# Performance work log

Measured on AMD Instinct MI355X. Metric: run time of the kernel, lower is better.

Reference implementation:

```python
import jax, jax.numpy as jnp
import numpy as np

B, T, D = 4, 1024, 1024
H, DK, DV = 4, 256, 512  # head_k_dim=256, head_v_dim=head_dim*expand_v=512
K_CONV = 4
EPS = 1e-5
L2_EPS = 1e-6


def silu(x):
    return x * jax.nn.sigmoid(x)


def causal_dw_conv(x, w):
    # x: [B,T,C], w: [C,K] depthwise causal conv (torch conv1d groups=C, left pad K-1)
    Kk = w.shape[1]
    xp = jnp.pad(x, ((0, 0), (Kk - 1, 0), (0, 0)))
    Tlen = x.shape[1]
    out = jnp.zeros_like(x)
    for i in range(Kk):
        out = out + xp[:, i:i + Tlen, :] * w[:, i]
    return out


def l2norm(x):
    return x * jax.lax.rsqrt(jnp.sum(x * x, axis=-1, keepdims=True) + L2_EPS)


def setup_inputs() -> dict:
    key = jax.random.key(0)
    ks = jax.random.split(key, 16)
    s = 0.02
    inp = {
        'x': jax.random.normal(ks[0], (B, T, D), jnp.float32),
        'Wq': jax.random.normal(ks[1], (D, H * DK), jnp.float32) * s,
        'Wk': jax.random.normal(ks[2], (D, H * DK), jnp.float32) * s,
        'Wv': jax.random.normal(ks[3], (D, H * DV), jnp.float32) * s,
        'conv_q_w': jax.random.normal(ks[4], (H * DK, K_CONV), jnp.float32) * 0.3,
        'conv_k_w': jax.random.normal(ks[5], (H * DK, K_CONV), jnp.float32) * 0.3,
        'conv_v_w': jax.random.normal(ks[6], (H * DV, K_CONV), jnp.float32) * 0.3,
        'Wb': jax.random.normal(ks[7], (D, H), jnp.float32) * s,
        'Wa': jax.random.normal(ks[8], (D, H), jnp.float32) * s,
        'A_log': jnp.log(jax.random.uniform(ks[9], (H,), jnp.float32, 1.0, 16.0)),
        'dt_bias': jax.random.normal(ks[10], (H,), jnp.float32) * 0.5,
        'Wg': jax.random.normal(ks[11], (D, H * DV), jnp.float32) * s,
        'norm_w': jnp.ones((DV,), jnp.float32),
        'Wo': jax.random.normal(ks[12], (H * DV, D), jnp.float32) * s,
    }
    return inp


def _forward(x, Wq, Wk, Wv, conv_q_w, conv_k_w, conv_v_w, Wb, Wa, A_log, dt_bias, Wg, norm_w, Wo):
    # projections + causal short conv + silu
    q = silu(causal_dw_conv(x @ Wq, conv_q_w)).reshape(B, T, H, DK)
    k = silu(causal_dw_conv(x @ Wk, conv_k_w)).reshape(B, T, H, DK)
    v = silu(causal_dw_conv(x @ Wv, conv_v_w)).reshape(B, T, H, DV)
    beta = jax.nn.sigmoid(x @ Wb)                                  # [B,T,H]
    g = -jnp.exp(A_log) * jax.nn.softplus(x @ Wa + dt_bias)        # [B,T,H]
    q = l2norm(q)
    k = l2norm(k)
    scale = DK ** -0.5

    # gated delta rule recurrence over time (state S: [B,H,DK,DV])
    qt = jnp.moveaxis(q, 1, 0)
    kt = jnp.moveaxis(k, 1, 0)
    vt = jnp.moveaxis(v, 1, 0)
    gt = jnp.moveaxis(g, 1, 0)
    bt = jnp.moveaxis(beta, 1, 0)

    S0 = jnp.zeros((B, H, DK, DV), x.dtype)

    def step(S, inps):
        q_t, k_t, v_t, g_t, b_t = inps
        S = S * jnp.exp(g_t)[..., None, None]
        kv = jnp.einsum('bhk,bhkv->bhv', k_t, S)
        delta = (v_t - kv) * b_t[..., None]
        S = S + jnp.einsum('bhk,bhv->bhkv', k_t, delta)
        o_t = jnp.einsum('bhk,bhkv->bhv', q_t * scale, S)
        return S, o_t

    _, o = jax.lax.scan(step, S0, (qt, kt, vt, gt, bt))
    o = jnp.moveaxis(o, 0, 1)                                      # [B,T,H,DV]

    # gated RMSNorm: rmsnorm(o) * weight * silu(gate)
    gate = (x @ Wg).reshape(B, T, H, DV)
    o = o * jax.lax.rsqrt(jnp.mean(o * o, axis=-1, keepdims=True) + EPS)
    o = o * norm_w * silu(gate)

    return o.reshape(B, T, H * DV) @ Wo


def reference(x, Wq, Wk, Wv, conv_q_w, conv_k_w, conv_v_w, Wb, Wa, A_log, dt_bias, Wg, norm_w, Wo):
    return _forward(x, Wq, Wk, Wv, conv_q_w, conv_k_w, conv_v_w, Wb, Wa, A_log, dt_bias, Wg, norm_w, Wo)
```

## Files before the change

kernel.cpp:

```cpp
#include <hip/hip_runtime.h>
#include <hip/hip_bf16.h>
#include <math.h>

#define B_ 4
#define T_ 1024
#define D_ 1024
#define H_ 4
#define DK_ 256
#define DV_ 512
#define KC_ 4

typedef __attribute__((ext_vector_type(4))) float floatx4;
typedef __attribute__((ext_vector_type(8))) short short8_t;

__device__ __forceinline__ unsigned short f2b(float f) {
    __hip_bfloat16 h = __float2bfloat16(f);
    return *(unsigned short*)&h;
}
__device__ __forceinline__ float b2f(unsigned short u) {
    unsigned int x = ((unsigned int)u) << 16;
    return *(float*)&x;
}

__global__ __launch_bounds__(256) void tob16_kernel(const float* __restrict__ in,
                                                    unsigned short* __restrict__ out) {
    int i = blockIdx.x * 256 + threadIdx.x;
    float4 f = ((const float4*)in)[i];
    ushort4 u;
    u.x = f2b(f.x); u.y = f2b(f.y); u.z = f2b(f.z); u.w = f2b(f.w);
    ((ushort4*)out)[i] = u;
}

__global__ __launch_bounds__(256) void transpose_bf16_kernel(const float* __restrict__ W,
                                                             unsigned short* __restrict__ Wt,
                                                             int K, int N) {
    __shared__ float Ls[32][33];
    int tx = threadIdx.x & 31, ty = threadIdx.x >> 5;
    int k0 = blockIdx.y * 32, n0 = blockIdx.x * 32;
#pragma unroll
    for (int i = 0; i < 4; ++i)
        Ls[ty * 4 + i][tx] = W[(size_t)(k0 + ty * 4 + i) * N + n0 + tx];
    __syncthreads();
#pragma unroll
    for (int i = 0; i < 4; ++i)
        Wt[(size_t)(n0 + ty * 4 + i) * K + k0 + tx] = f2b(Ls[tx][ty * 4 + i]);
}

__global__ __launch_bounds__(256) void gemm_bf16_kernel(const unsigned short* __restrict__ A,
                                                        const unsigned short* __restrict__ Bt,
                                                        float* __restrict__ C,
                                                        int M, int N, int K) {
    __shared__ unsigned short As[128 * 40];
    __shared__ unsigned short Bs[128 * 40];
    int tid = threadIdx.x;
    int m0 = blockIdx.y * 128, n0 = blockIdx.x * 128;
    int w = tid >> 6, lane = tid & 63;
    int wm = w >> 1, wn = w & 1;
    floatx4 acc[4][4] = {};

    int c0 = tid, c1 = 256 + tid;
    int r0 = c0 >> 2, col0 = (c0 & 3) * 8;
    int r1 = c1 >> 2, col1 = (c1 & 3) * 8;
    int koff = (lane >> 4) * 8;

    for (int k0 = 0; k0 < K; k0 += 32) {
        short8_t a0 = *(const short8_t*)&A[(size_t)(m0 + r0) * K + k0 + col0];
        short8_t a1 = *(const short8_t*)&A[(size_t)(m0 + r1) * K + k0 + col1];
        short8_t b0 = *(const short8_t*)&Bt[(size_t)(n0 + r0) * K + k0 + col0];
        short8_t b1 = *(const short8_t*)&Bt[(size_t)(n0 + r1) * K + k0 + col1];
        __syncthreads();
        *(short8_t*)&As[r0 * 40 + col0] = a0;
        *(short8_t*)&As[r1 * 40 + col1] = a1;
        *(short8_t*)&Bs[r0 * 40 + col0] = b0;
        *(short8_t*)&Bs[r1 * 40 + col1] = b1;
        __syncthreads();
        short8_t af[4], bf[4];
#pragma unroll
        for (int f = 0; f < 4; ++f) {
            af[f] = *(const short8_t*)&As[(wm * 64 + f * 16 + (lane & 15)) * 40 + koff];
            bf[f] = *(const short8_t*)&Bs[(wn * 64 + f * 16 + (lane & 15)) * 40 + koff];
        }
#pragma unroll
        for (int i = 0; i < 4; ++i)
#pragma unroll
            for (int j = 0; j < 4; ++j)
                acc[i][j] = __builtin_amdgcn_mfma_f32_16x16x32_bf16(af[i], bf[j], acc[i][j], 0, 0, 0);
    }
#pragma unroll
    for (int i = 0; i < 4; ++i) {
        int row = m0 + wm * 64 + i * 16 + (lane >> 4) * 4;
#pragma unroll
        for (int j = 0; j < 4; ++j) {
            int col = n0 + wn * 64 + j * 16 + (lane & 15);
#pragma unroll
            for (int r = 0; r < 4; ++r)
                C[(size_t)(row + r) * N + col] = acc[i][j][r];
        }
    }
}

__global__ __launch_bounds__(256) void betag_kernel(const float* __restrict__ x,
                                                    const float* __restrict__ Wb,
                                                    const float* __restrict__ Wa,
                                                    const float* __restrict__ A_log,
                                                    const float* __restrict__ dt_bias,
                                                    float* __restrict__ beta,
                                                    float* __restrict__ g) {
    int row = blockIdx.x;
    int tid = threadIdx.x;
    const float* xr = x + (size_t)row * D_;
    float pb[H_] = {}, pa[H_] = {};
    for (int j = 0; j < D_ / 256; ++j) {
        int d = j * 256 + tid;
        float xv = xr[d];
#pragma unroll
        for (int h = 0; h < H_; ++h) {
            pb[h] = fmaf(xv, Wb[d * H_ + h], pb[h]);
            pa[h] = fmaf(xv, Wa[d * H_ + h], pa[h]);
        }
    }
#pragma unroll
    for (int h = 0; h < H_; ++h) {
        for (int off = 32; off; off >>= 1) {
            pb[h] += __shfl_down(pb[h], off);
            pa[h] += __shfl_down(pa[h], off);
        }
    }
    __shared__ float ws[4][2][H_];
    int lane = tid & 63, w = tid >> 6;
    if (lane == 0) {
#pragma unroll
        for (int h = 0; h < H_; ++h) {
            ws[w][0][h] = pb[h];
            ws[w][1][h] = pa[h];
        }
    }
    __syncthreads();
    if (tid < H_) {
        float db = ws[0][0][tid] + ws[1][0][tid] + ws[2][0][tid] + ws[3][0][tid];
        float da = ws[0][1][tid] + ws[1][1][tid] + ws[2][1][tid] + ws[3][1][tid];
        beta[(size_t)row * H_ + tid] = 1.f / (1.f + expf(-db));
        float z = da + dt_bias[tid];
        float sp = (z > 20.f) ? z : log1pf(expf(z));
        g[(size_t)row * H_ + tid] = -expf(A_log[tid]) * sp;
    }
}

__global__ __launch_bounds__(256) void convqk_kernel(const float* __restrict__ raw,
                                                     const float* __restrict__ w,
                                                     __hip_bfloat16* __restrict__ out) {
    int bt_h = blockIdx.x;
    int h = bt_h & (H_ - 1);
    int row = bt_h >> 2;
    int t = row & (T_ - 1);
    int c = threadIdx.x;
    int C = h * DK_ + c;
    float acc = 0.f;
#pragma unroll
    for (int i = 0; i < KC_; ++i) {
        int tt = t - (KC_ - 1) + i;
        if (tt >= 0)
            acc = fmaf(raw[(size_t)(row - (KC_ - 1) + i) * (H_ * DK_) + C], w[C * KC_ + i], acc);
    }
    float s = acc / (1.f + expf(-acc));
    float ss = s * s;
    for (int off = 32; off; off >>= 1) ss += __shfl_down(ss, off);
    __shared__ float ws4[4];
    int lane = threadIdx.x & 63, wv = threadIdx.x >> 6;
    if (lane == 0) ws4[wv] = ss;
    __syncthreads();
    float tot = ws4[0] + ws4[1] + ws4[2] + ws4[3];
    float r = rsqrtf(tot + 1e-6f);
    out[(size_t)bt_h * DK_ + c] = __float2bfloat16(s * r);
}

__global__ __launch_bounds__(256) void convv_kernel(const float* __restrict__ raw,
                                                    const float* __restrict__ w,
                                                    __hip_bfloat16* __restrict__ out) {
    size_t idx = (size_t)blockIdx.x * 256 + threadIdx.x;
    int C = idx & (H_ * DV_ - 1);
    int row = (int)(idx >> 11);
    int t = row & (T_ - 1);
    float acc = 0.f;
#pragma unroll
    for (int i = 0; i < KC_; ++i) {
        int tt = t - (KC_ - 1) + i;
        if (tt >= 0)
            acc = fmaf(raw[(size_t)(row - (KC_ - 1) + i) * (H_ * DV_) + C], w[C * KC_ + i], acc);
    }
    out[idx] = __float2bfloat16(acc / (1.f + expf(-acc)));
}

__global__ __launch_bounds__(256) void prep_kernel(const unsigned short* __restrict__ qn,
                                                   const unsigned short* __restrict__ kn,
                                                   const float* __restrict__ gl,
                                                   const float* __restrict__ betal,
                                                   float* __restrict__ Afg,
                                                   unsigned short* __restrict__ KdTg,
                                                   unsigned short* __restrict__ Pg,
                                                   float* __restrict__ lambg,
                                                   float* __restrict__ scl0,
                                                   float* __restrict__ scl1) {
    int blk = blockIdx.x;
    int nc = blk & 31, bh = blk >> 5;
    int b = bh >> 2, h = bh & 3;
    int t0 = nc * 32;
    int tid = threadIdx.x, w = tid >> 6, l = tid & 63;
    int vl = l & 15, hq = l >> 4;
    size_t cb = (size_t)bh * 32 + nc;

    __shared__ __align__(16) unsigned short Kt[32][264];
    __shared__ float gcs[32], bets[32], kdec[32];

    if (tid < 32) {
        size_t base = ((size_t)(b * T_ + t0 + tid) * H_ + h);
        float gv = gl[base];
        float bv = betal[base];
        float x = gv;
#pragma unroll
        for (int off = 1; off < 32; off <<= 1) {
            float y = __shfl_up(x, off);
            if (tid >= off) x += y;
        }
        gcs[tid] = x;
        float lm = expf(x);
        bets[tid] = bv;
        float tot = __shfl(x, 31);
        kdec[tid] = expf(tot - x);
        lambg[cb * 32 + tid] = lm;
        scl0[cb * 32 + tid] = bv * lm;
        scl1[cb * 32 + tid] = bv;
    }
    __syncthreads();
    {
        int r = tid >> 3, c8 = (tid & 7) * 32;
        size_t gbase = ((size_t)(b * T_ + t0 + r) * H_ + h) * DK_;
#pragma unroll
        for (int ii = 0; ii < 4; ++ii)
            *(short8_t*)&Kt[r][c8 + ii * 8] = *(const short8_t*)&kn[gbase + c8 + ii * 8];
    }
    __syncthreads();
    if (w < 3) {
        int mt = (w == 0) ? 0 : 1;
        int nt = (w == 2) ? 1 : 0;
        floatx4 acc = {};
#pragma unroll
        for (int k0 = 0; k0 < 8; ++k0) {
            short8_t a = *(const short8_t*)&Kt[mt * 16 + vl][k0 * 32 + hq * 8];
            short8_t bb = *(const short8_t*)&Kt[nt * 16 + vl][k0 * 32 + hq * 8];
            acc = __builtin_amdgcn_mfma_f32_16x16x32_bf16(a, bb, acc, 0, 0, 0);
        }
#pragma unroll
        for (int r = 0; r < 4; ++r) {
            int i = mt * 16 + 4 * hq + r, j = nt * 16 + vl;
            Afg[cb * 1024 + i * 32 + j] = (j < i) ? bets[i] * expf(gcs[i] - gcs[j]) * acc[r] : 0.f;
        }
        floatx4 accp = {};
#pragma unroll
        for (int k0 = 0; k0 < 8; ++k0) {
            size_t qrow = ((size_t)(b * T_ + t0 + mt * 16 + vl) * H_ + h) * DK_ + k0 * 32 + hq * 8;
            short8_t a = *(const short8_t*)&qn[qrow];
            short8_t bb = *(const short8_t*)&Kt[nt * 16 + vl][k0 * 32 + hq * 8];
            accp = __builtin_amdgcn_mfma_f32_16x16x32_bf16(a, bb, accp, 0, 0, 0);
        }
#pragma unroll
        for (int r = 0; r < 4; ++r) {
            int i = mt * 16 + 4 * hq + r, j = nt * 16 + vl;
            Pg[cb * 1024 + i * 32 + j] = f2b((j <= i) ? expf(gcs[i] - gcs[j]) * accp[r] : 0.f);
        }
    } else {
#pragma unroll
        for (int ii = 0; ii < 4; ++ii)
            Pg[cb * 1024 + (l >> 2) * 32 + 16 + (l & 3) * 4 + ii] = 0;
    }
    {
#pragma unroll
        for (int it = 0; it < 16; ++it) {
            int uidx = it * 256 + tid;
            int k = uidx >> 4, cp = (uidx & 15) * 2;
            float kv0 = b2f(Kt[cp][k]) * kdec[cp];
            float kv1 = b2f(Kt[cp + 1][k]) * kdec[cp + 1];
            unsigned int pk = (unsigned int)f2b(kv0) | ((unsigned int)f2b(kv1) << 16);
            ((unsigned int*)KdTg)[cb * 4096 + uidx] = pk;
        }
    }
}

__global__ __launch_bounds__(256) void solve_kernel(const unsigned short* __restrict__ kn,
                                                    const unsigned short* __restrict__ vn,
                                                    const float* __restrict__ Afg,
                                                    const float* __restrict__ scl0,
                                                    const float* __restrict__ scl1,
                                                    unsigned short* __restrict__ Wpg,
                                                    unsigned short* __restrict__ Ug) {
    int part = blockIdx.x;
    int cbi = blockIdx.y;
    int bh = cbi >> 5, nc = cbi & 31;
    int b = bh >> 2, h = bh & 3;
    int t0 = nc * 32;
    int tid = threadIdx.x;

    __shared__ float Af[32][33];
    __shared__ float s0[32];
#pragma unroll
    for (int i = 0; i < 4; ++i) {
        int e = i * 256 + tid;
        Af[e >> 5][e & 31] = Afg[(size_t)cbi * 1024 + e];
    }
    if (tid < 32)
        s0[tid] = (part == 0) ? scl0[(size_t)cbi * 32 + tid] : scl1[(size_t)cbi * 32 + tid];
    __syncthreads();

    float u[32];
    if (part == 0) {
#pragma unroll
        for (int r = 0; r < 32; ++r)
            u[r] = s0[r] * b2f(kn[((size_t)(b * T_ + t0 + r) * H_ + h) * DK_ + tid]);
    } else {
        int col = (part - 1) * 256 + tid;
#pragma unroll
        for (int r = 0; r < 32; ++r)
            u[r] = s0[r] * b2f(vn[((size_t)(b * T_ + t0 + r) * H_ + h) * DV_ + col]);
    }
#pragma unroll
    for (int r = 1; r < 32; ++r) {
        float a = 0.f;
#pragma unroll
        for (int l2 = 0; l2 < r; ++l2)
            a = fmaf(Af[r][l2], u[l2], a);
        u[r] -= a;
    }
    if (part == 0) {
#pragma unroll
        for (int r = 0; r < 32; ++r)
            Wpg[(size_t)cbi * 8192 + r * 256 + tid] = f2b(u[r]);
    } else {
        int col = (part - 1) * 256 + tid;
#pragma unroll
        for (int r = 0; r < 32; ++r)
            Ug[((size_t)cbi * 32 + r) * 512 + col] = f2b(u[r]);
    }
}

__global__ __launch_bounds__(256) void seq_kernel(const unsigned short* __restrict__ qn,
                                                  const unsigned short* __restrict__ Wpg,
                                                  const unsigned short* __restrict__ KdTg,
                                                  const unsigned short* __restrict__ Pg,
                                                  const unsigned short* __restrict__ Ug,
                                                  const float* __restrict__ lambg,
                                                  float* __restrict__ o) {
    int blk = blockIdx.x;
    int vg = blk & 31, bh = blk >> 5;
    int b = bh >> 2, h = bh & 3;
    int tid = threadIdx.x;
    int w = tid >> 6, l = tid & 63;
    int vl = l & 15, hq = l >> 4;
    int v0 = vg * 16;

    __shared__ float Pu[4][32][17];
    __shared__ float Po[4][32][17];
    __shared__ __align__(16) unsigned short Ru[16][40];
    __shared__ float R2[4][64][17];

    float S[2][8] = {};

    for (int nc = 0; nc < 32; ++nc) {
        size_t cb = (size_t)bh * 32 + nc;
        int t0 = nc * 32;
        int ur_row = 8 * w + 2 * hq;
        float Ur0 = b2f(Ug[(cb * 32 + ur_row) * 512 + v0 + vl]);
        float Ur1 = b2f(Ug[(cb * 32 + ur_row + 1) * 512 + v0 + vl]);
        float lamC = lambg[cb * 32 + 31];
        float lmb[4];
        if (w < 2) {
#pragma unroll
            for (int r = 0; r < 4; ++r)
                lmb[r] = lambg[cb * 32 + 16 * w + 4 * hq + r];
        }
        short8_t bhi[2], blo[2];
#pragma unroll
        for (int kt = 0; kt < 2; ++kt)
#pragma unroll
            for (int j = 0; j < 8; ++j) {
                float sv = S[kt][j];
                unsigned short hh = f2b(sv);
                bhi[kt][j] = (short)hh;
                blo[kt][j] = (short)f2b(sv - b2f(hh));
            }
        floatx4 ua0 = {}, ua1 = {}, oa0 = {}, oa1 = {};
        const unsigned short* Wpc = Wpg + cb * 8192;
#pragma unroll
        for (int kt = 0; kt < 2; ++kt) {
            int kofs = w * 64 + kt * 32 + hq * 8;
            short8_t wa0 = *(const short8_t*)&Wpc[vl * 256 + kofs];
            short8_t wa1 = *(const short8_t*)&Wpc[(16 + vl) * 256 + kofs];
            short8_t qa0 = *(const short8_t*)&qn[((size_t)(b * T_ + t0 + vl) * H_ + h) * DK_ + kofs];
            short8_t qa1 = *(const short8_t*)&qn[((size_t)(b * T_ + t0 + 16 + vl) * H_ + h) * DK_ + kofs];
            ua0 = __builtin_amdgcn_mfma_f32_16x16x32_bf16(wa0, bhi[kt], ua0, 0, 0, 0);
            ua0 = __builtin_amdgcn_mfma_f32_16x16x32_bf16(wa0, blo[kt], ua0, 0, 0, 0);
            ua1 = __builtin_amdgcn_mfma_f32_16x16x32_bf16(wa1, bhi[kt], ua1, 0, 0, 0);
            ua1 = __builtin_amdgcn_mfma_f32_16x16x32_bf16(wa1, blo[kt], ua1, 0, 0, 0);
            oa0 = __builtin_amdgcn_mfma_f32_16x16x32_bf16(qa0, bhi[kt], oa0, 0, 0, 0);
            oa0 = __builtin_amdgcn_mfma_f32_16x16x32_bf16(qa0, blo[kt], oa0, 0, 0, 0);
            oa1 = __builtin_amdgcn_mfma_f32_16x16x32_bf16(qa1, bhi[kt], oa1, 0, 0, 0);
            oa1 = __builtin_amdgcn_mfma_f32_16x16x32_bf16(qa1, blo[kt], oa1, 0, 0, 0);
        }
#pragma unroll
        for (int r = 0; r < 4; ++r) {
            Pu[w][4 * hq + r][vl] = ua0[r];
            Pu[w][16 + 4 * hq + r][vl] = ua1[r];
            Po[w][4 * hq + r][vl] = oa0[r];
            Po[w][16 + 4 * hq + r][vl] = oa1[r];
        }
        __syncthreads();
#pragma unroll
        for (int j = 0; j < 2; ++j) {
            int r = ur_row + j;
            float s = Pu[0][r][vl] + Pu[1][r][vl] + Pu[2][r][vl] + Pu[3][r][vl];
            Ru[vl][r] = f2b(((j == 0) ? Ur0 : Ur1) - s);
        }
        __syncthreads();
        short8_t uf = *(const short8_t*)&Ru[vl][8 * hq];
        if (w < 2) {
            short8_t p = *(const short8_t*)&Pg[cb * 1024 + (w * 16 + vl) * 32 + hq * 8];
            floatx4 pa = {};
            pa = __builtin_amdgcn_mfma_f32_16x16x32_bf16(p, uf, pa, 0, 0, 0);
#pragma unroll
            for (int r = 0; r < 4; ++r) {
                int row = 16 * w + 4 * hq + r;
                float po = Po[0][row][vl] + Po[1][row][vl] + Po[2][row][vl] + Po[3][row][vl];
                o[((size_t)(b * T_ + t0 + row) * H_ + h) * DV_ + v0 + vl] =
                    0.0625f * (lmb[r] * po + pa[r]);
            }
        }
        const unsigned short* Kc = KdTg + cb * 8192;
#pragma unroll
        for (int kt = 0; kt < 4; ++kt) {
            short8_t ka = *(const short8_t*)&Kc[(w * 64 + kt * 16 + vl) * 32 + hq * 8];
            floatx4 sa = {};
            sa = __builtin_amdgcn_mfma_f32_16x16x32_bf16(ka, uf, sa, 0, 0, 0);
#pragma unroll
            for (int r = 0; r < 4; ++r)
                R2[w][kt * 16 + 4 * hq + r][vl] = sa[r];
        }
#pragma unroll
        for (int kt = 0; kt < 2; ++kt)
#pragma unroll
            for (int j = 0; j < 8; ++j)
                S[kt][j] = fmaf(lamC, S[kt][j], R2[w][kt * 32 + hq * 8 + j][vl]);
        __syncthreads();
    }
}

__global__ __launch_bounds__(256) void gnorm_kernel(const float* __restrict__ o,
                                                    const float* __restrict__ gate,
                                                    const float* __restrict__ norm_w,
                                                    __hip_bfloat16* __restrict__ on) {
    int bth = blockIdx.x;
    int tid = threadIdx.x;
    const float* orow = o + (size_t)bth * DV_;
    float v0 = orow[tid], v1 = orow[256 + tid];
    float ss = v0 * v0 + v1 * v1;
    for (int off = 32; off; off >>= 1) ss += __shfl_down(ss, off);
    __shared__ float ws4[4];
    int lane = tid & 63, wv = tid >> 6;
    if (lane == 0) ws4[wv] = ss;
    __syncthreads();
    float tot = ws4[0] + ws4[1] + ws4[2] + ws4[3];
    float r = rsqrtf(tot * (1.f / DV_) + 1e-5f);
    float g0 = gate[(size_t)bth * DV_ + tid];
    float g1 = gate[(size_t)bth * DV_ + 256 + tid];
    on[(size_t)bth * DV_ + tid] = __float2bfloat16(v0 * r * norm_w[tid] * (g0 / (1.f + expf(-g0))));
    on[(size_t)bth * DV_ + 256 + tid] = __float2bfloat16(v1 * r * norm_w[256 + tid] * (g1 / (1.f + expf(-g1))));
}

extern "C" void kernel_launch(void* const* d_in, const int* in_sizes, int n_in,
                              void* d_out, int out_size, void* d_ws, size_t ws_size,
                              hipStream_t stream) {
    const float* x = (const float*)d_in[0];
    const float* Wq = (const float*)d_in[1];
    const float* Wk = (const float*)d_in[2];
    const float* Wv = (const float*)d_in[3];
    const float* cqw = (const float*)d_in[4];
    const float* ckw = (const float*)d_in[5];
    const float* cvw = (const float*)d_in[6];
    const float* Wb = (const float*)d_in[7];
    const float* Wa = (const float*)d_in[8];
    const float* A_log = (const float*)d_in[9];
    const float* dt_bias = (const float*)d_in[10];
    const float* Wg = (const float*)d_in[11];
    const float* norm_w = (const float*)d_in[12];
    const float* Wo = (const float*)d_in[13];
    float* out = (float*)d_out;

    float* ws = (float*)d_ws;
    const size_t M1 = (size_t)1024 * 1024;
    float* qraw = ws;
    float* kraw = ws + 4 * M1;
    float* vraw = ws + 8 * M1;
    float* graw = ws + 8 * M1;
    unsigned short* qn = (unsigned short*)(ws + 16 * M1);
    unsigned short* kn = (unsigned short*)(ws + 18 * M1);
    unsigned short* vn = (unsigned short*)(ws + 20 * M1);
    float* g = ws + 24 * M1;
    float* beta = g + 16384;
    unsigned short* Ug = (unsigned short*)ws;
    float* lambg = ws + 4 * M1;
    unsigned short* Pg = (unsigned short*)(ws + 4 * M1 + 16384);
    float* Afg = ws + 5 * M1;
    float* scl0 = ws + 5 * M1 + M1 / 2;
    float* scl1 = scl0 + 16384;
    float* o = ws + 18 * M1;
    unsigned short* xb = (unsigned short*)(ws + 25 * M1);
    unsigned short* WqT = (unsigned short*)(ws + 27 * M1);
    unsigned short* WkT = (unsigned short*)(ws + 27 * M1 + M1 / 2);
    unsigned short* WvT = (unsigned short*)(ws + 28 * M1);
    unsigned short* WgT = (unsigned short*)(ws + 29 * M1);
    unsigned short* WoT = (unsigned short*)(ws + 30 * M1);
    unsigned short* Wpg = (unsigned short*)(ws + 26 * M1);
    unsigned short* KdTg = (unsigned short*)(ws + 28 * M1);
    __hip_bfloat16* onb = (__hip_bfloat16*)(ws + 16 * M1);

    dim3 blk(256);
    tob16_kernel<<<4096, blk, 0, stream>>>(x, xb);
    transpose_bf16_kernel<<<dim3(32, 32), blk, 0, stream>>>(Wq, WqT, 1024, 1024);
    transpose_bf16_kernel<<<dim3(32, 32), blk, 0, stream>>>(Wk, WkT, 1024, 1024);
    transpose_bf16_kernel<<<dim3(64, 32), blk, 0, stream>>>(Wv, WvT, 1024, 2048);
    transpose_bf16_kernel<<<dim3(64, 32), blk, 0, stream>>>(Wg, WgT, 1024, 2048);
    transpose_bf16_kernel<<<dim3(32, 64), blk, 0, stream>>>(Wo, WoT, 2048, 1024);
    gemm_bf16_kernel<<<dim3(8, 32), blk, 0, stream>>>(xb, WqT, qraw, 4096, 1024, 1024);
    gemm_bf16_kernel<<<dim3(8, 32), blk, 0, stream>>>(xb, WkT, kraw, 4096, 1024, 1024);
    gemm_bf16_kernel<<<dim3(16, 32), blk, 0, stream>>>(xb, WvT, vraw, 4096, 2048, 1024);
    betag_kernel<<<4096, blk, 0, stream>>>(x, Wb, Wa, A_log, dt_bias, beta, g);
    convqk_kernel<<<16384, blk, 0, stream>>>(qraw, cqw, (__hip_bfloat16*)qn);
    convqk_kernel<<<16384, blk, 0, stream>>>(kraw, ckw, (__hip_bfloat16*)kn);
    convv_kernel<<<32768, blk, 0, stream>>>(vraw, cvw, (__hip_bfloat16*)vn);
    gemm_bf16_kernel<<<dim3(16, 32), blk, 0, stream>>>(xb, WgT, graw, 4096, 2048, 1024);
    prep_kernel<<<512, blk, 0, stream>>>(qn, kn, g, beta, Afg, KdTg, Pg, lambg, scl0, scl1);
    solve_kernel<<<dim3(3, 512), blk, 0, stream>>>(kn, vn, Afg, scl0, scl1, Wpg, Ug);
    seq_kernel<<<512, blk, 0, stream>>>(qn, Wpg, KdTg, Pg, Ug, lambg, o);
    gnorm_kernel<<<16384, blk, 0, stream>>>(o, graw, norm_w, onb);
    gemm_bf16_kernel<<<dim3(8, 32), blk, 0, stream>>>((const unsigned short*)onb, WoT, out, 4096, 1024, 2048);
}
```

Measured before the change: 618.1 us.

## Fuse Q/K/V projections into one GEMM, store recurrence output as bf16

The Wq, Wk and Wv transposes are written into one concatenated weight, so a single 4096-wide GEMM replaces three separate projection GEMMs. The conv kernels now take a row stride so they can read their slices of the combined output. The recurrence output is stored as bf16 and the gated norm rewrites it in place, which halves that intermediate's traffic and drops a buffer. solve_kernel also gets a launch-bounds occupancy hint, and the workspace layout is reshuffled. The risk is a small precision loss from rounding the recurrence output to bf16 before the norm.

```diff
diff --git a/kernel.cpp b/kernel.cpp
--- a/kernel.cpp
+++ b/kernel.cpp
@@ -147,6 +147,7 @@
 }
 
 __global__ __launch_bounds__(256) void convqk_kernel(const float* __restrict__ raw,
+                                                     int stride,
                                                      const float* __restrict__ w,
                                                      __hip_bfloat16* __restrict__ out) {
     int bt_h = blockIdx.x;
@@ -160,7 +161,7 @@
     for (int i = 0; i < KC_; ++i) {
         int tt = t - (KC_ - 1) + i;
         if (tt >= 0)
-            acc = fmaf(raw[(size_t)(row - (KC_ - 1) + i) * (H_ * DK_) + C], w[C * KC_ + i], acc);
+            acc = fmaf(raw[(size_t)(row - (KC_ - 1) + i) * stride + C], w[C * KC_ + i], acc);
     }
     float s = acc / (1.f + expf(-acc));
     float ss = s * s;
@@ -175,6 +176,7 @@
 }
 
 __global__ __launch_bounds__(256) void convv_kernel(const float* __restrict__ raw,
+                                                    int stride,
                                                     const float* __restrict__ w,
                                                     __hip_bfloat16* __restrict__ out) {
     size_t idx = (size_t)blockIdx.x * 256 + threadIdx.x;
@@ -186,7 +188,7 @@
     for (int i = 0; i < KC_; ++i) {
         int tt = t - (KC_ - 1) + i;
         if (tt >= 0)
-            acc = fmaf(raw[(size_t)(row - (KC_ - 1) + i) * (H_ * DV_) + C], w[C * KC_ + i], acc);
+            acc = fmaf(raw[(size_t)(row - (KC_ - 1) + i) * stride + C], w[C * KC_ + i], acc);
     }
     out[idx] = __float2bfloat16(acc / (1.f + expf(-acc)));
 }
@@ -286,13 +288,13 @@
     }
 }
 
-__global__ __launch_bounds__(256) void solve_kernel(const unsigned short* __restrict__ kn,
-                                                    const unsigned short* __restrict__ vn,
-                                                    const float* __restrict__ Afg,
-                                                    const float* __restrict__ scl0,
-                                                    const float* __restrict__ scl1,
-                                                    unsigned short* __restrict__ Wpg,
-                                                    unsigned short* __restrict__ Ug) {
+__global__ __launch_bounds__(256, 4) void solve_kernel(const unsigned short* __restrict__ kn,
+                                                       const unsigned short* __restrict__ vn,
+                                                       const float* __restrict__ Afg,
+                                                       const float* __restrict__ scl0,
+                                                       const float* __restrict__ scl1,
+                                                       unsigned short* __restrict__ Wpg,
+                                                       unsigned short* __restrict__ Ug) {
     int part = blockIdx.x;
     int cbi = blockIdx.y;
     int bh = cbi >> 5, nc = cbi & 31;
@@ -348,7 +350,7 @@
                                                   const unsigned short* __restrict__ Pg,
                                                   const unsigned short* __restrict__ Ug,
                                                   const float* __restrict__ lambg,
-                                                  float* __restrict__ o) {
+                                                  unsigned short* __restrict__ o) {
     int blk = blockIdx.x;
     int vg = blk & 31, bh = blk >> 5;
     int b = bh >> 2, h = bh & 3;
@@ -430,7 +432,7 @@
                 int row = 16 * w + 4 * hq + r;
                 float po = Po[0][row][vl] + Po[1][row][vl] + Po[2][row][vl] + Po[3][row][vl];
                 o[((size_t)(b * T_ + t0 + row) * H_ + h) * DV_ + v0 + vl] =
-                    0.0625f * (lmb[r] * po + pa[r]);
+                    f2b(0.0625f * (lmb[r] * po + pa[r]));
             }
         }
         const unsigned short* Kc = KdTg + cb * 8192;
@@ -452,14 +454,13 @@
     }
 }
 
-__global__ __launch_bounds__(256) void gnorm_kernel(const float* __restrict__ o,
+__global__ __launch_bounds__(256) void gnorm_kernel(unsigned short* __restrict__ o,
                                                     const float* __restrict__ gate,
-                                                    const float* __restrict__ norm_w,
-                                                    __hip_bfloat16* __restrict__ on) {
+                                                    const float* __restrict__ norm_w) {
     int bth = blockIdx.x;
     int tid = threadIdx.x;
-    const float* orow = o + (size_t)bth * DV_;
-    float v0 = orow[tid], v1 = orow[256 + tid];
+    unsigned short* orow = o + (size_t)bth * DV_;
+    float v0 = b2f(orow[tid]), v1 = b2f(orow[256 + tid]);
     float ss = v0 * v0 + v1 * v1;
     for (int off = 32; off; off >>= 1) ss += __shfl_down(ss, off);
     __shared__ float ws4[4];
@@ -470,8 +471,8 @@
     float r = rsqrtf(tot * (1.f / DV_) + 1e-5f);
     float g0 = gate[(size_t)bth * DV_ + tid];
     float g1 = gate[(size_t)bth * DV_ + 256 + tid];
-    on[(size_t)bth * DV_ + tid] = __float2bfloat16(v0 * r * norm_w[tid] * (g0 / (1.f + expf(-g0))));
-    on[(size_t)bth * DV_ + 256 + tid] = __float2bfloat16(v1 * r * norm_w[256 + tid] * (g1 / (1.f + expf(-g1))));
+    orow[tid] = f2b(v0 * r * norm_w[tid] * (g0 / (1.f + expf(-g0))));
+    orow[256 + tid] = f2b(v1 * r * norm_w[256 + tid] * (g1 / (1.f + expf(-g1))));
 }
 
 extern "C" void kernel_launch(void* const* d_in, const int* in_sizes, int n_in,
@@ -495,50 +496,43 @@
 
     float* ws = (float*)d_ws;
     const size_t M1 = (size_t)1024 * 1024;
-    float* qraw = ws;
-    float* kraw = ws + 4 * M1;
-    float* vraw = ws + 8 * M1;
-    float* graw = ws + 8 * M1;
-    unsigned short* qn = (unsigned short*)(ws + 16 * M1);
-    unsigned short* kn = (unsigned short*)(ws + 18 * M1);
-    unsigned short* vn = (unsigned short*)(ws + 20 * M1);
-    float* g = ws + 24 * M1;
+    float* praw = ws;
+    float* graw = ws;
+    unsigned short* xb = (unsigned short*)(ws + 16 * M1);
+    unsigned short* WcatT = (unsigned short*)(ws + 18 * M1);
+    unsigned short* WgT = (unsigned short*)(ws + 20 * M1);
+    unsigned short* WoT = (unsigned short*)(ws + 21 * M1);
+    unsigned short* qn = (unsigned short*)(ws + 22 * M1);
+    unsigned short* kn = (unsigned short*)(ws + 24 * M1);
+    unsigned short* vn = (unsigned short*)(ws + 26 * M1);
+    float* g = ws + 30 * M1;
     float* beta = g + 16384;
-    unsigned short* Ug = (unsigned short*)ws;
-    float* lambg = ws + 4 * M1;
-    unsigned short* Pg = (unsigned short*)(ws + 4 * M1 + 16384);
-    float* Afg = ws + 5 * M1;
-    float* scl0 = ws + 5 * M1 + M1 / 2;
+    float* Afg = ws + 8 * M1;
+    unsigned short* Pg = (unsigned short*)(ws + 8 * M1 + M1 / 2);
+    unsigned short* KdTg = (unsigned short*)(ws + 9 * M1);
+    float* lambg = ws + 11 * M1;
+    float* scl0 = lambg + 16384;
     float* scl1 = scl0 + 16384;
-    float* o = ws + 18 * M1;
-    unsigned short* xb = (unsigned short*)(ws + 25 * M1);
-    unsigned short* WqT = (unsigned short*)(ws + 27 * M1);
-    unsigned short* WkT = (unsigned short*)(ws + 27 * M1 + M1 / 2);
-    unsigned short* WvT = (unsigned short*)(ws + 28 * M1);
-    unsigned short* WgT = (unsigned short*)(ws + 29 * M1);
-    unsigned short* WoT = (unsigned short*)(ws + 30 * M1);
-    unsigned short* Wpg = (unsigned short*)(ws + 26 * M1);
-    unsigned short* KdTg = (unsigned short*)(ws + 28 * M1);
-    __hip_bfloat16* onb = (__hip_bfloat16*)(ws + 16 * M1);
+    unsigned short* Wpg = (unsigned short*)(ws + 12 * M1);
+    unsigned short* Ug = (unsigned short*)(ws + 14 * M1);
+    unsigned short* ob = (unsigned short*)(ws + 24 * M1);
 
     dim3 blk(256);
     tob16_kernel<<<4096, blk, 0, stream>>>(x, xb);
-    transpose_bf16_kernel<<<dim3(32, 32), blk, 0, stream>>>(Wq, WqT, 1024, 1024);
-    transpose_bf16_kernel<<<dim3(32, 32), blk, 0, stream>>>(Wk, WkT, 1024, 1024);
-    transpose_bf16_kernel<<<dim3(64, 32), blk, 0, stream>>>(Wv, WvT, 1024, 2048);
+    transpose_bf16_kernel<<<dim3(32, 32), blk, 0, stream>>>(Wq, WcatT, 1024, 1024);
+    transpose_bf16_kernel<<<dim3(32, 32), blk, 0, stream>>>(Wk, WcatT + (size_t)1024 * 1024, 1024, 1024);
+    transpose_bf16_kernel<<<dim3(64, 32), blk, 0, stream>>>(Wv, WcatT + (size_t)2048 * 1024, 1024, 2048);
     transpose_bf16_kernel<<<dim3(64, 32), blk, 0, stream>>>(Wg, WgT, 1024, 2048);
     transpose_bf16_kernel<<<dim3(32, 64), blk, 0, stream>>>(Wo, WoT, 2048, 1024);
-    gemm_bf16_kernel<<<dim3(8, 32), blk, 0, stream>>>(xb, WqT, qraw, 4096, 1024, 1024);
-    gemm_bf16_kernel<<<dim3(8, 32), blk, 0, stream>>>(xb, WkT, kraw, 4096, 1024, 1024);
-    gemm_bf16_kernel<<<dim3(16, 32), blk, 0, stream>>>(xb, WvT, vraw, 4096, 2048, 1024);
+    gemm_bf16_kernel<<<dim3(32, 32), blk, 0, stream>>>(xb, WcatT, praw, 4096, 4096, 1024);
     betag_kernel<<<4096, blk, 0, stream>>>(x, Wb, Wa, A_log, dt_bias, beta, g);
-    convqk_kernel<<<16384, blk, 0, stream>>>(qraw, cqw, (__hip_bfloat16*)qn);
-    convqk_kernel<<<16384, blk, 0, stream>>>(kraw, ckw, (__hip_bfloat16*)kn);
-    convv_kernel<<<32768, blk, 0, stream>>>(vraw, cvw, (__hip_bfloat16*)vn);
+    convqk_kernel<<<16384, blk, 0, stream>>>(praw, 4096, cqw, (__hip_bfloat16*)qn);
+    convqk_kernel<<<16384, blk, 0, stream>>>(praw + 1024, 4096, ckw, (__hip_bfloat16*)kn);
+    convv_kernel<<<32768, blk, 0, stream>>>(praw + 2048, 4096, cvw, (__hip_bfloat16*)vn);
     gemm_bf16_kernel<<<dim3(16, 32), blk, 0, stream>>>(xb, WgT, graw, 4096, 2048, 1024);
     prep_kernel<<<512, blk, 0, stream>>>(qn, kn, g, beta, Afg, KdTg, Pg, lambg, scl0, scl1);
     solve_kernel<<<dim3(3, 512), blk, 0, stream>>>(kn, vn, Afg, scl0, scl1, Wpg, Ug);
-    seq_kernel<<<512, blk, 0, stream>>>(qn, Wpg, KdTg, Pg, Ug, lambg, o);
-    gnorm_kernel<<<16384, blk, 0, stream>>>(o, graw, norm_w, onb);
-    gemm_bf16_kernel<<<dim3(8, 32), blk, 0, stream>>>((const unsigned short*)onb, WoT, out, 4096, 1024, 2048);
-}
+    seq_kernel<<<512, blk, 0, stream>>>(qn, Wpg, KdTg, Pg, Ug, lambg, ob);
+    gnorm_kernel<<<16384, blk, 0, stream>>>(ob, graw, norm_w);
+    gemm_bf16_kernel<<<dim3(8, 32), blk, 0, stream>>>(ob, WoT, out, 4096, 1024, 2048);
+}
```

Result: slower. 893.4 us (+44.5%).
